# Kernel tuning notes

Hardware: AMD Instinct MI355X
Metric: run time of the kernel (lower is better)

The kernel has to match this reference:

```python
import jax, jax.numpy as jnp
import numpy as np

HEADS = 8

def setup_inputs() -> dict:
    key = jax.random.key(0)
    ks = jax.random.split(key, 11)
    B, S, E = 4, 2048, 512
    sc = 1.0 / np.sqrt(E)
    return {
        "inputs": jax.random.normal(ks[0], (B, S, E), jnp.float32),
        "entangle": jax.random.uniform(ks[1], (S,), jnp.float32),
        "Wq": jax.random.normal(ks[2], (E, E), jnp.float32) * sc,
        "bq": jax.random.normal(ks[3], (E,), jnp.float32) * 0.01,
        "Wk": jax.random.normal(ks[4], (E, E), jnp.float32) * sc,
        "bk": jax.random.normal(ks[5], (E,), jnp.float32) * 0.01,
        "Wv": jax.random.normal(ks[6], (E, E), jnp.float32) * sc,
        "bv": jax.random.normal(ks[7], (E,), jnp.float32) * 0.01,
        "Wo": jax.random.normal(ks[8], (E, E), jnp.float32) * sc,
        "bo": jax.random.normal(ks[9], (E,), jnp.float32) * 0.01,
    }

def reference(inputs, entangle, Wq, bq, Wk, bk, Wv, bv, Wo, bo):
    B, S, E = inputs.shape
    H = HEADS
    D = E // H
    # torch nn.Linear: y = x @ W.T + b
    Q = (inputs @ Wq.T + bq).reshape(B, S, H, D)
    K = (inputs @ Wk.T + bk).reshape(B, S, H, D)
    V = (inputs @ Wv.T + bv).reshape(B, S, H, D)
    scores = jnp.einsum('bqhd,bkhd->bhqk', Q, K) / jnp.sqrt(jnp.float32(D))
    # entangle broadcast as (1,1,S,1): per-query-position scaling before softmax
    scores = scores * entangle[None, None, :, None]
    attn = jax.nn.softmax(scores, axis=-1)
    out = jnp.einsum('bhqk,bkhd->bqhd', attn, V).reshape(B, S, E)
    return out @ Wo.T + bo
```

## Files before the change

kernel.cpp:

```cpp
#include <hip/hip_runtime.h>
#include <hip/hip_bf16.h>

#define BB 4
#define SS 2048
#define EE 512
#define HH 8
#define DD 64

typedef __attribute__((ext_vector_type(8))) short bf16x8;
typedef __attribute__((ext_vector_type(4))) float f32x4;
typedef __attribute__((ext_vector_type(4))) unsigned int u32x4;

__device__ __forceinline__ unsigned short f2bf(float f) {
    __hip_bfloat16 h = __float2bfloat16(f);
    return *reinterpret_cast<unsigned short*>(&h);
}

__device__ __forceinline__ unsigned int cvtpk(float lo, float hi) {
    unsigned int r;
    asm("v_cvt_pk_bf16_f32 %0, %1, %2" : "=v"(r) : "v"(lo), "v"(hi));
    return r;
}

__device__ __forceinline__ void pl32(unsigned int& a, unsigned int& b) {
    asm("v_permlane32_swap_b32 %0, %1" : "+v"(a), "+v"(b));
}
__device__ __forceinline__ void pl16(unsigned int& a, unsigned int& b) {
    asm("v_permlane16_swap_b32 %0, %1" : "+v"(a), "+v"(b));
}

__device__ __forceinline__ void gll16(const unsigned short* g, unsigned short* l) {
    __builtin_amdgcn_global_load_lds(
        (const __attribute__((address_space(1))) unsigned int*)g,
        (__attribute__((address_space(3))) unsigned int*)l,
        16, 0, 0);
}

__global__ __launch_bounds__(256)
void cast_all(const float* __restrict__ x,
              const float* __restrict__ wq, const float* __restrict__ wk,
              const float* __restrict__ wv, const float* __restrict__ wo,
              unsigned short* __restrict__ xb,
              unsigned short* __restrict__ wqb, unsigned short* __restrict__ wkb,
              unsigned short* __restrict__ wvb, unsigned short* __restrict__ wob)
{
    const int bid = blockIdx.x;
    const float* src; unsigned short* dst; int lb;
    if (bid < 4096)      { src = x;  dst = xb;  lb = bid; }
    else {
        const int t = (bid - 4096) >> 8;
        lb = (bid - 4096) & 255;
        switch (t) {
            case 0:  src = wq; dst = wqb; break;
            case 1:  src = wk; dst = wkb; break;
            case 2:  src = wv; dst = wvb; break;
            default: src = wo; dst = wob; break;
        }
    }
    const int i = lb * 256 + threadIdx.x;
    const float4 v = reinterpret_cast<const float4*>(src)[i];
    ushort4 o;
    o.x = f2bf(v.x); o.y = f2bf(v.y); o.z = f2bf(v.z); o.w = f2bf(v.w);
    reinterpret_cast<ushort4*>(dst)[i] = o;
}

template<typename OutT, bool TRANSPOSE_V, int TM>
__global__ __launch_bounds__(256)
void gemm_mfma_nt(const unsigned short* __restrict__ A,
                  const unsigned short* __restrict__ W0, const float* __restrict__ b0, OutT* __restrict__ C0,
                  const unsigned short* __restrict__ W1, const float* __restrict__ b1, OutT* __restrict__ C1,
                  const unsigned short* __restrict__ W2, const float* __restrict__ b2, OutT* __restrict__ C2,
                  const float* __restrict__ rowscale,
                  int M, int N, int K)
{
    const unsigned short* W = (blockIdx.z == 0) ? W0 : (blockIdx.z == 1) ? W1 : W2;
    const float* bias       = (blockIdx.z == 0) ? b0 : (blockIdx.z == 1) ? b1 : b2;
    OutT* C                 = (blockIdx.z == 0) ? C0 : (blockIdx.z == 1) ? C1 : C2;

    constexpr int MT = TM / 32;
    __shared__ unsigned short As[2][TM * 32];
    __shared__ unsigned short Bs[2][128 * 32];

    const int tid  = threadIdx.x;
    const int wave = tid >> 6, lane = tid & 63;
    const int quad = lane >> 4, r16 = lane & 15;
    const int m0 = blockIdx.x * TM, n0 = blockIdx.y * 128;
    const int wm0 = (wave >> 1) * (TM / 2), wn0 = (wave & 1) * 64;

    f32x4 acc[MT][4];
    const f32x4 zero = {0.f, 0.f, 0.f, 0.f};
    #pragma unroll
    for (int i = 0; i < MT; ++i)
        #pragma unroll
        for (int j = 0; j < 4; ++j) acc[i][j] = zero;

    const int swz = (r16 >> 1) & 3;

    auto stage = [&](int bi, int k0) {
        #pragma unroll
        for (int j = 0; j < TM / 64; ++j) {
            const int cb = wave * 64 + j * 256;
            const int c  = cb + lane;
            const int row = c >> 2, cc = (c & 3) ^ ((row >> 1) & 3);
            gll16(&A[(size_t)(m0 + row) * K + k0 + cc * 8], &As[bi][cb * 8]);
        }
        #pragma unroll
        for (int j = 0; j < 2; ++j) {
            const int cb = wave * 64 + j * 256;
            const int c  = cb + lane;
            const int row = c >> 2, cc = (c & 3) ^ ((row >> 1) & 3);
            gll16(&W[(size_t)(n0 + row) * K + k0 + cc * 8], &Bs[bi][cb * 8]);
        }
    };

    stage(0, 0);

    const int NI = K / 32;
    for (int i = 0; i < NI; ++i) {
        const int cur = i & 1;
        __syncthreads();
        if (i + 1 < NI) stage(cur ^ 1, (i + 1) * 32);

        bf16x8 af[MT], bfr[4];
        #pragma unroll
        for (int t = 0; t < MT; ++t)
            af[t]  = *reinterpret_cast<bf16x8*>(&As[cur][((wm0 + t * 16 + r16) * 4 + (quad ^ swz)) * 8]);
        #pragma unroll
        for (int t = 0; t < 4; ++t)
            bfr[t] = *reinterpret_cast<bf16x8*>(&Bs[cur][((wn0 + t * 16 + r16) * 4 + (quad ^ swz)) * 8]);
        #pragma unroll
        for (int mt = 0; mt < MT; ++mt)
            #pragma unroll
            for (int nt = 0; nt < 4; ++nt)
                acc[mt][nt] = __builtin_amdgcn_mfma_f32_16x16x32_bf16(
                    af[mt], bfr[nt], acc[mt][nt], 0, 0, 0);
    }

    if (TRANSPOSE_V && blockIdx.z == 2) {
        #pragma unroll
        for (int mt = 0; mt < MT; ++mt) {
            const int m = m0 + wm0 + mt * 16 + quad * 4;
            const int bb = m >> 11, s0 = m & (SS - 1);
            #pragma unroll
            for (int nt = 0; nt < 4; ++nt) {
                const int col = n0 + wn0 + nt * 16 + r16;
                const float bv = bias[col];
                uint2 o;
                o.x = cvtpk(acc[mt][nt][0] + bv, acc[mt][nt][1] + bv);
                o.y = cvtpk(acc[mt][nt][2] + bv, acc[mt][nt][3] + bv);
                *reinterpret_cast<uint2*>(
                    &((unsigned short*)C2)[(size_t)bb * EE * SS + (size_t)col * SS + s0]) = o;
            }
        }
        return;
    }
    const bool doscale = (rowscale != nullptr) && (blockIdx.z == 0);
    #pragma unroll
    for (int mt = 0; mt < MT; ++mt) {
        float rs[4];
        #pragma unroll
        for (int r = 0; r < 4; ++r) {
            const int row = m0 + wm0 + mt * 16 + quad * 4 + r;
            rs[r] = doscale ? rowscale[row & (SS - 1)] * 0.18033688f : 1.0f;
        }
        #pragma unroll
        for (int nt = 0; nt < 4; ++nt) {
            const int col = n0 + wn0 + nt * 16 + r16;
            const float bv = bias[col];
            #pragma unroll
            for (int r = 0; r < 4; ++r) {
                const int row = m0 + wm0 + mt * 16 + quad * 4 + r;
                const float v = (acc[mt][nt][r] + bv) * rs[r];
                if constexpr (sizeof(OutT) == 2)
                    C[(size_t)row * N + col] = (OutT)f2bf(v);
                else
                    C[(size_t)row * N + col] = (OutT)v;
            }
        }
    }
}

#define QBLK 128

__global__ __launch_bounds__(256)
void attn_mfma(const unsigned short* __restrict__ Q,
               const unsigned short* __restrict__ K,
               const unsigned short* __restrict__ Vt,
               unsigned short* __restrict__ O)
{
    __shared__ unsigned short Ks[3][72 * 64];
    __shared__ unsigned short Vs[3][72 * 64];

    const int tid  = threadIdx.x;
    const int wave = tid >> 6, lane = tid & 63;
    const int quad = lane >> 4, r16 = lane & 15;
    const int h  = blockIdx.x;
    const int q0 = blockIdx.y * QBLK;
    const int b  = blockIdx.z;
    const size_t base    = (size_t)b * SS * EE + (size_t)h * DD;
    const size_t base_vt = ((size_t)b * HH + h) * DD * SS;

    bf16x8 qf[2][2];
    #pragma unroll
    for (int s = 0; s < 2; ++s) {
        const int qrow = q0 + s * 64 + wave * 16 + r16;
        #pragma unroll
        for (int dh = 0; dh < 2; ++dh)
            qf[s][dh] = *reinterpret_cast<const bf16x8*>(
                &Q[base + (size_t)qrow * EE + dh * 32 + quad * 8]);
    }

    const int cb0 = wave * 64, cb1 = wave * 64 + 256;
    const int c0 = cb0 + lane, c1 = cb1 + lane;
    const int row0 = c0 >> 3, cc0 = (c0 & 7) ^ (row0 & 7);
    const int row1 = c1 >> 3, cc1 = (c1 & 7) ^ (row1 & 7);
    const unsigned short* kp0 = &K[base + (size_t)row0 * EE + cc0 * 8];
    const unsigned short* kp1 = &K[base + (size_t)row1 * EE + cc1 * 8];
    const unsigned short* vp0 = &Vt[base_vt + (size_t)row0 * SS + cc0 * 8];
    const unsigned short* vp1 = &Vt[base_vt + (size_t)row1 * SS + cc1 * 8];

    auto stage = [&](int bi, int kt) {
        const size_t ko = (size_t)kt * 64 * EE;
        const int    vo = kt * 64;
        gll16(kp0 + ko, &Ks[bi][cb0 * 8]);
        gll16(vp0 + vo, &Vs[bi][cb0 * 8]);
        gll16(kp1 + ko, &Ks[bi][cb1 * 8]);
        gll16(vp1 + vo, &Vs[bi][cb1 * 8]);
    };

    float l_lane[2] = {0.f, 0.f};
    f32x4 o_acc[2][4];
    const f32x4 zero = {0.f, 0.f, 0.f, 0.f};
    #pragma unroll
    for (int s = 0; s < 2; ++s)
        #pragma unroll
        for (int dt = 0; dt < 4; ++dt) o_acc[s][dt] = zero;

    const int swz = r16 & 7;

    stage(0, 0);
    stage(1, 1);

    constexpr int NT = SS / 64;
    for (int kt = 0; kt < NT; ++kt) {
        const int cur = kt % 3;
        if (kt + 1 < NT) asm volatile("s_waitcnt vmcnt(4)" ::: "memory");
        else             asm volatile("s_waitcnt vmcnt(0)" ::: "memory");
        __builtin_amdgcn_s_barrier();
        __builtin_amdgcn_sched_barrier(0);
        if (kt + 2 < NT) stage((kt + 2) % 3, kt + 2);

        const unsigned short* Kc = &Ks[cur][0];
        const unsigned short* Vc = &Vs[cur][0];

        bf16x8 kfA[4], kfB[4];
        #pragma unroll
        for (int tn = 0; tn < 4; ++tn) {
            kfA[tn] = *reinterpret_cast<const bf16x8*>(&Kc[((tn * 16 + r16) * 8 + (quad ^ swz)) * 8]);
            kfB[tn] = *reinterpret_cast<const bf16x8*>(&Kc[((tn * 16 + r16) * 8 + ((quad + 4) ^ swz)) * 8]);
        }

        f32x4 st[2][4];
        #pragma unroll
        for (int s = 0; s < 2; ++s)
            #pragma unroll
            for (int tn = 0; tn < 4; ++tn) st[s][tn] = zero;
        #pragma unroll
        for (int s = 0; s < 2; ++s)
            #pragma unroll
            for (int tn = 0; tn < 4; ++tn) {
                st[s][tn] = __builtin_amdgcn_mfma_f32_16x16x32_bf16(kfA[tn], qf[s][0], st[s][tn], 0, 0, 0);
                st[s][tn] = __builtin_amdgcn_mfma_f32_16x16x32_bf16(kfB[tn], qf[s][1], st[s][tn], 0, 0, 0);
            }

        bf16x8 vfA[4], vfB[4];
        #pragma unroll
        for (int dt = 0; dt < 4; ++dt) {
            vfA[dt] = *reinterpret_cast<const bf16x8*>(&Vc[((dt * 16 + r16) * 8 + (quad ^ swz)) * 8]);
            vfB[dt] = *reinterpret_cast<const bf16x8*>(&Vc[((dt * 16 + r16) * 8 + ((quad + 4) ^ swz)) * 8]);
        }

        #pragma unroll
        for (int s = 0; s < 2; ++s) {
            unsigned int w[4][2];
            #pragma unroll
            for (int tn = 0; tn < 4; ++tn) {
                const float p0 = exp2f(st[s][tn][0]);
                const float p1 = exp2f(st[s][tn][1]);
                const float p2 = exp2f(st[s][tn][2]);
                const float p3 = exp2f(st[s][tn][3]);
                l_lane[s] += (p0 + p1) + (p2 + p3);
                w[tn][0] = cvtpk(p0, p1);
                w[tn][1] = cvtpk(p2, p3);
            }
            unsigned int pa0 = w[0][0], pa2 = w[1][0];
            pl32(pa0, pa2); pl16(pa0, pa2);
            unsigned int pa1 = w[0][1], pa3 = w[1][1];
            pl32(pa1, pa3); pl16(pa1, pa3);
            unsigned int pb0 = w[2][0], pb2 = w[3][0];
            pl32(pb0, pb2); pl16(pb0, pb2);
            unsigned int pb1 = w[2][1], pb3 = w[3][1];
            pl32(pb1, pb3); pl16(pb1, pb3);

            const u32x4 ua = {pa0, pa1, pa2, pa3};
            const u32x4 ub = {pb0, pb1, pb2, pb3};
            const bf16x8 pf0 = __builtin_bit_cast(bf16x8, ua);
            const bf16x8 pf1 = __builtin_bit_cast(bf16x8, ub);

            #pragma unroll
            for (int dt = 0; dt < 4; ++dt) {
                o_acc[s][dt] = __builtin_amdgcn_mfma_f32_16x16x32_bf16(pf0, vfA[dt], o_acc[s][dt], 0, 0, 0);
                o_acc[s][dt] = __builtin_amdgcn_mfma_f32_16x16x32_bf16(pf1, vfB[dt], o_acc[s][dt], 0, 0, 0);
            }
        }
    }

    #pragma unroll
    for (int s = 0; s < 2; ++s) {
        float l = l_lane[s];
        l += __shfl_xor(l, 16, 64);
        l += __shfl_xor(l, 32, 64);
        #pragma unroll
        for (int r = 0; r < 4; ++r) {
            const float il = 1.0f / __shfl(l, quad * 4 + r, 64);
            const int q = q0 + s * 64 + wave * 16 + quad * 4 + r;
            #pragma unroll
            for (int dt = 0; dt < 4; ++dt)
                O[base + (size_t)q * EE + dt * 16 + r16] = f2bf(o_acc[s][dt][r] * il);
        }
    }
}

extern "C" void kernel_launch(void* const* d_in, const int* in_sizes, int n_in,
                              void* d_out, int out_size, void* d_ws, size_t ws_size,
                              hipStream_t stream) {
    const float* x   = (const float*)d_in[0];
    const float* ent = (const float*)d_in[1];
    const float* Wq  = (const float*)d_in[2];
    const float* bq  = (const float*)d_in[3];
    const float* Wk  = (const float*)d_in[4];
    const float* bk  = (const float*)d_in[5];
    const float* Wv  = (const float*)d_in[6];
    const float* bv  = (const float*)d_in[7];
    const float* Wo  = (const float*)d_in[8];
    const float* bo  = (const float*)d_in[9];
    float* out = (float*)d_out;

    const size_t n_x = (size_t)BB * SS * EE;
    const size_t n_w = (size_t)EE * EE;

    unsigned short* xb  = (unsigned short*)d_ws;
    unsigned short* wqb = xb + n_x;
    unsigned short* wkb = wqb + n_w;
    unsigned short* wvb = wkb + n_w;
    unsigned short* wob = wvb + n_w;
    unsigned short* Qb  = wob + n_w;
    unsigned short* Kb  = Qb + n_x;
    unsigned short* Vtb = Kb + n_x;
    unsigned short* AOb = Vtb + n_x;

    const int M = BB * SS;

    dim3 gc(4096 + 4 * 256, 1, 1);
    cast_all<<<gc, 256, 0, stream>>>(x, Wq, Wk, Wv, Wo, xb, wqb, wkb, wvb, wob);

    dim3 gq(M / 128, EE / 128, 3);
    gemm_mfma_nt<unsigned short, true, 128><<<gq, 256, 0, stream>>>(
        xb, wqb, bq, Qb, wkb, bk, Kb, wvb, bv, Vtb, ent, M, EE, EE);

    dim3 ga(HH, SS / QBLK, BB);
    attn_mfma<<<ga, 256, 0, stream>>>(Qb, Kb, Vtb, AOb);

    dim3 go(M / 64, EE / 128, 1);
    gemm_mfma_nt<float, false, 64><<<go, 256, 0, stream>>>(
        AOb, wob, bo, out, wob, bo, out, wob, bo, out, nullptr, M, EE, EE);
}
```

Measured before the change: 192.8 us.

## Triple-buffer GEMM loads, add MFMA priority hints, use raw v_exp_f32

The projection GEMM moves from double to triple-buffered LDS staging with explicit vmcnt waits and a raw s_barrier, so loads run two K-steps ahead. The attention kernel raises wave priority around its MFMA blocks with s_setprio. It also swaps exp2f for a raw v_exp_f32, dropping the range handling the library call adds. The costs are more LDS per block, which can lower occupancy, and hand-counted waitcnt values that must exactly match the number of loads issued per stage.

```diff
diff --git a/kernel.cpp b/kernel.cpp
--- a/kernel.cpp
+++ b/kernel.cpp
@@ -19,6 +19,12 @@
 __device__ __forceinline__ unsigned int cvtpk(float lo, float hi) {
     unsigned int r;
     asm("v_cvt_pk_bf16_f32 %0, %1, %2" : "=v"(r) : "v"(lo), "v"(hi));
+    return r;
+}
+
+__device__ __forceinline__ float ex2(float x) {
+    float r;
+    asm("v_exp_f32 %0, %1" : "=v"(r) : "v"(x));
     return r;
 }
 
@@ -78,8 +84,8 @@
     OutT* C                 = (blockIdx.z == 0) ? C0 : (blockIdx.z == 1) ? C1 : C2;
 
     constexpr int MT = TM / 32;
-    __shared__ unsigned short As[2][TM * 32];
-    __shared__ unsigned short Bs[2][128 * 32];
+    __shared__ unsigned short As[3][TM * 32];
+    __shared__ unsigned short Bs[3][128 * 32];
 
     const int tid  = threadIdx.x;
     const int wave = tid >> 6, lane = tid & 63;
@@ -114,12 +120,20 @@
     };
 
     stage(0, 0);
+    stage(1, 32);
 
     const int NI = K / 32;
     for (int i = 0; i < NI; ++i) {
-        const int cur = i & 1;
-        __syncthreads();
-        if (i + 1 < NI) stage(cur ^ 1, (i + 1) * 32);
+        const int cur = i % 3;
+        if (i + 1 < NI) {
+            if constexpr (TM == 128) asm volatile("s_waitcnt vmcnt(4)" ::: "memory");
+            else                     asm volatile("s_waitcnt vmcnt(3)" ::: "memory");
+        } else {
+            asm volatile("s_waitcnt vmcnt(0)" ::: "memory");
+        }
+        __builtin_amdgcn_s_barrier();
+        __builtin_amdgcn_sched_barrier(0);
+        if (i + 2 < NI) stage((i + 2) % 3, (i + 2) * 32);
 
         bf16x8 af[MT], bfr[4];
         #pragma unroll
@@ -265,6 +279,7 @@
         for (int s = 0; s < 2; ++s)
             #pragma unroll
             for (int tn = 0; tn < 4; ++tn) st[s][tn] = zero;
+        __builtin_amdgcn_s_setprio(1);
         #pragma unroll
         for (int s = 0; s < 2; ++s)
             #pragma unroll
@@ -272,6 +287,7 @@
                 st[s][tn] = __builtin_amdgcn_mfma_f32_16x16x32_bf16(kfA[tn], qf[s][0], st[s][tn], 0, 0, 0);
                 st[s][tn] = __builtin_amdgcn_mfma_f32_16x16x32_bf16(kfB[tn], qf[s][1], st[s][tn], 0, 0, 0);
             }
+        __builtin_amdgcn_s_setprio(0);
 
         bf16x8 vfA[4], vfB[4];
         #pragma unroll
@@ -285,10 +301,10 @@
             unsigned int w[4][2];
             #pragma unroll
             for (int tn = 0; tn < 4; ++tn) {
-                const float p0 = exp2f(st[s][tn][0]);
-                const float p1 = exp2f(st[s][tn][1]);
-                const float p2 = exp2f(st[s][tn][2]);
-                const float p3 = exp2f(st[s][tn][3]);
+                const float p0 = ex2(st[s][tn][0]);
+                const float p1 = ex2(st[s][tn][1]);
+                const float p2 = ex2(st[s][tn][2]);
+                const float p3 = ex2(st[s][tn][3]);
                 l_lane[s] += (p0 + p1) + (p2 + p3);
                 w[tn][0] = cvtpk(p0, p1);
                 w[tn][1] = cvtpk(p2, p3);
@@ -307,11 +323,13 @@
             const bf16x8 pf0 = __builtin_bit_cast(bf16x8, ua);
             const bf16x8 pf1 = __builtin_bit_cast(bf16x8, ub);
 
+            __builtin_amdgcn_s_setprio(1);
             #pragma unroll
             for (int dt = 0; dt < 4; ++dt) {
                 o_acc[s][dt] = __builtin_amdgcn_mfma_f32_16x16x32_bf16(pf0, vfA[dt], o_acc[s][dt], 0, 0, 0);
                 o_acc[s][dt] = __builtin_amdgcn_mfma_f32_16x16x32_bf16(pf1, vfB[dt], o_acc[s][dt], 0, 0, 0);
             }
+            __builtin_amdgcn_s_setprio(0);
         }
     }
 
```

Result: faster. 180.7 us (-6.3%).
